# Optimization experiments

Measured on AMD Instinct MI355X. Metric: run time of the kernel, lower is better.

Reference implementation:

```python
import jax, jax.numpy as jnp
import numpy as np

WS = 2   # window_size
NH = 8   # num_heads


def window_attn(x, Wqkv, bqkv, scale, ws=WS, nh=NH):
    # x: (B, H, W, C) -> tiny ws*ws-token windowed MHA, faithful to torch reshape order
    B, H, W, C = x.shape
    hg, wg = H // ws, W // ws
    hd = C // nh
    xw = x.reshape(B, hg, ws, wg, ws, C).transpose(0, 1, 3, 2, 4, 5)  # (B,hg,wg,ws,ws,C)
    qkv = (xw @ Wqkv + bqkv).reshape(B, hg * wg, ws * ws, 3, nh, hd)
    q, k, v = jnp.transpose(qkv, (3, 0, 1, 4, 2, 5))  # each (B,G,nh,n,hd), n=ws*ws
    attn = jax.nn.softmax(jnp.einsum('bgnqd,bgnkd->bgnqk', q, k) * scale, axis=-1)
    o = jnp.einsum('bgnqk,bgnkd->bgnqd', attn, v)
    o = o.transpose(0, 1, 3, 2, 4).reshape(B, hg, wg, ws, ws, C)
    return o.transpose(0, 1, 3, 2, 4, 5).reshape(B, H, W, C)


def reference(x, Wqkv, bqkv, Wproj, bproj):
    B, C, H, W = x.shape
    scale = (C // NH) ** (-0.5)
    xr = x.reshape(B, H, W, C)  # raw reshape (NOT a transpose) -- faithful to source

    # --- Global path ---
    g = window_attn(xr, Wqkv, bqkv, scale) @ Wproj + bproj

    # --- Local path ---
    l = xr.reshape(B, C, H, W)                         # raw reshape, as in source
    l = l.reshape(B, C, H // 2, 2, W // 2, 2).mean(axis=(3, 5))  # AvgPool2d(2)
    h, w = H // 2, W // 2
    l = l.reshape(B, h, w, C)                          # raw reshape, as in source
    l = window_attn(l, Wqkv, bqkv, scale)
    l = l.reshape(B, C, h, w)                          # raw reshape, as in source
    # attn_x: reflect-pad top by 1, AvgPool2d((2,1), stride=1)
    px = jnp.pad(l, ((0, 0), (0, 0), (1, 0), (0, 0)), mode='reflect')
    lx = 0.5 * (px[:, :, :-1, :] + px[:, :, 1:, :])
    # attn_y: reflect-pad right by 1, AvgPool2d((1,2), stride=1)
    py = jnp.pad(l, ((0, 0), (0, 0), (0, 0), (0, 1)), mode='reflect')
    ly = 0.5 * (py[..., :-1] + py[..., 1:])
    # bilinear upsample x2, align_corners=False (half-pixel, matches jax.image.resize)
    l = jax.image.resize(lx + ly, (B, C, H, W), method='bilinear')
    l = l.reshape(B, H, W, C)                          # raw reshape, as in source

    return (g + l).transpose(0, 3, 1, 2)  # (B, C, H, W)


def setup_inputs() -> dict:
    key = jax.random.key(0)
    k1, k2, k3, k4, k5 = jax.random.split(key, 5)
    B, C, H, W = 4, 512, 128, 128
    x = jax.random.normal(k1, (B, C, H, W), dtype=jnp.float32)
    Wqkv = jax.random.normal(k2, (C, 3 * C), dtype=jnp.float32) * 0.02
    bqkv = jax.random.normal(k3, (3 * C,), dtype=jnp.float32) * 0.02
    Wproj = jax.random.normal(k4, (C, C), dtype=jnp.float32) * 0.02
    bproj = jax.random.normal(k5, (C,), dtype=jnp.float32) * 0.02
    return {'x': x, 'Wqkv': Wqkv, 'bqkv': bqkv, 'Wproj': Wproj, 'bproj': bproj}
```

## Files before the change

kernel.cpp:

```cpp
#include <hip/hip_runtime.h>

typedef float f32x4 __attribute__((ext_vector_type(4)));
typedef float f32x2 __attribute__((ext_vector_type(2)));
typedef __bf16 bf16x8 __attribute__((ext_vector_type(8)));
typedef __bf16 bf16x4 __attribute__((ext_vector_type(4)));

__device__ __forceinline__ void gll16(const void* g, void* l) {
  __builtin_amdgcn_global_load_lds(
      (const __attribute__((address_space(1))) uint32_t*)g,
      (__attribute__((address_space(3))) uint32_t*)l, 16, 0, 0);
}

__global__ __launch_bounds__(256) void gemm_bf16_k512(
    const __bf16* __restrict__ A, const __bf16* __restrict__ BT,
    const float* __restrict__ bias, __bf16* __restrict__ C, int N, int gx)
{
  __shared__ __bf16 As[2][8192];
  __shared__ __bf16 Bs[2][8192];
  const int tid = threadIdx.x;
  const int wave = tid >> 6, lane = tid & 63;
  const int wr = (wave >> 1) * 64, wc = (wave & 1) * 64;
  const int l15 = lane & 15, l4 = lane >> 4;

  int lin = blockIdx.x;
  int olin = (lin & 7) * ((int)gridDim.x >> 3) + (lin >> 3);
  int bn = olin % gx, bm = olin / gx;
  const long arow0 = (long)bm * 128;
  const long brow0 = (long)bn * 128;

  const int srow = wave * 8 + (lane >> 3);
  const int scp8 = (lane & 7) * 8;

  f32x4 acc[4][4] = {};

  auto stage = [&](int p, int kt) {
    #pragma unroll
    for (int i = 0; i < 4; i++) {
      int row = srow + i * 32;
      int gc = scp8 ^ ((row & 7) * 8);
      gll16(A  + (arow0 + row) * 512 + kt + gc, (char*)As[p] + i * 4096 + wave * 1024);
      gll16(BT + (brow0 + row) * 512 + kt + gc, (char*)Bs[p] + i * 4096 + wave * 1024);
    }
  };

  stage(0, 0);
  __syncthreads();

  for (int t = 0; t < 8; t++) {
    int cur = t & 1;
    if (t < 7) stage(cur ^ 1, (t + 1) * 64);
    #pragma unroll
    for (int kk = 0; kk < 2; kk++) {
      bf16x8 af[4], bfr[4];
      #pragma unroll
      for (int m = 0; m < 4; m++) {
        int row = wr + m * 16 + l15;
        int cp8 = ((kk * 4 + l4) * 8) ^ ((row & 7) * 8);
        af[m] = *(const bf16x8*)&As[cur][row * 64 + cp8];
      }
      #pragma unroll
      for (int n = 0; n < 4; n++) {
        int row = wc + n * 16 + l15;
        int cp8 = ((kk * 4 + l4) * 8) ^ ((row & 7) * 8);
        bfr[n] = *(const bf16x8*)&Bs[cur][row * 64 + cp8];
      }
      #pragma unroll
      for (int m = 0; m < 4; m++)
        #pragma unroll
        for (int n = 0; n < 4; n++)
          acc[m][n] = __builtin_amdgcn_mfma_f32_16x16x32_bf16(bfr[n], af[m], acc[m][n], 0, 0, 0);
    }
    if (t < 7) __syncthreads();
  }

  #pragma unroll
  for (int m = 0; m < 4; m++) {
    long row = arow0 + wr + m * 16 + l15;
    __bf16* crow = C + row * (long)N + brow0;
    #pragma unroll
    for (int n = 0; n < 4; n++) {
      f32x4 bv = *(const f32x4*)(bias + brow0 + wc + n * 16 + l4 * 4);
      bf16x4 o;
      #pragma unroll
      for (int k = 0; k < 4; k++) o[k] = (__bf16)(acc[m][n][k] + bv[k]);
      *(bf16x4*)(crow + wc + n * 16 + l4 * 4) = o;
    }
  }
}

__global__ __launch_bounds__(256) void attn4(
    const __bf16* __restrict__ qkv, __bf16* __restrict__ o,
    int nwin, int wg, int Wimg, int wpb, int bst)
{
  int tid = blockIdx.x * 256 + threadIdx.x;
  int m = tid & 3;
  int head = (tid >> 2) & 7;
  int win = tid >> 5;
  if (win >= nwin) return;
  int b = win / wpb, wrm = win % wpb;
  int i = wrm / wg, j = wrm % wg;
  int t0 = b * bst + 2 * i * Wimg + 2 * j;
  int tn[4] = { t0, t0 + 1, t0 + Wimg, t0 + Wimg + 1 };
  int trow = tn[m];
  const int co = head * 64;

  float qf[64];
  #pragma unroll
  for (int c = 0; c < 8; c++) {
    bf16x8 v = *(const bf16x8*)(qkv + (long)trow * 1536 + co + c * 8);
    #pragma unroll
    for (int e = 0; e < 8; e++) qf[c * 8 + e] = (float)v[e];
  }

  float s[4];
  #pragma unroll
  for (int n = 0; n < 4; n++) {
    float acc = 0.f;
    #pragma unroll
    for (int c = 0; c < 8; c++) {
      bf16x8 kv = *(const bf16x8*)(qkv + (long)tn[n] * 1536 + 512 + co + c * 8);
      #pragma unroll
      for (int e = 0; e < 8; e++) acc += qf[c * 8 + e] * (float)kv[e];
    }
    s[n] = acc * 0.125f;
  }

  float mx = fmaxf(fmaxf(s[0], s[1]), fmaxf(s[2], s[3]));
  float e0 = __expf(s[0] - mx), e1 = __expf(s[1] - mx),
        e2 = __expf(s[2] - mx), e3 = __expf(s[3] - mx);
  float inv = 1.f / (e0 + e1 + e2 + e3);
  float w4[4] = { e0 * inv, e1 * inv, e2 * inv, e3 * inv };

  float of[64] = {};
  #pragma unroll
  for (int n = 0; n < 4; n++) {
    float wn = w4[n];
    #pragma unroll
    for (int c = 0; c < 8; c++) {
      bf16x8 vv = *(const bf16x8*)(qkv + (long)tn[n] * 1536 + 1024 + co + c * 8);
      #pragma unroll
      for (int e = 0; e < 8; e++) of[c * 8 + e] += wn * (float)vv[e];
    }
  }

  #pragma unroll
  for (int c = 0; c < 8; c++) {
    bf16x8 ov;
    #pragma unroll
    for (int e = 0; e < 8; e++) ov[e] = (__bf16)of[c * 8 + e];
    *(bf16x8*)(o + (long)trow * 512 + co + c * 8) = ov;
  }
}

__global__ __launch_bounds__(256) void transpose_f32_bf16(
    const float* __restrict__ in, __bf16* __restrict__ out, int K, int N)
{
  __shared__ float t[64][65];
  int n0 = blockIdx.x * 64, k0 = blockIdx.y * 64;
  int tid = threadIdx.x;
  int nl4 = (tid & 15) * 4, kl = tid >> 4;
  #pragma unroll
  for (int p = 0; p < 4; p++) {
    int kk = kl + p * 16;
    f32x4 v = *(const f32x4*)(in + (long)(k0 + kk) * N + n0 + nl4);
    t[kk][nl4 + 0] = v.x; t[kk][nl4 + 1] = v.y; t[kk][nl4 + 2] = v.z; t[kk][nl4 + 3] = v.w;
  }
  __syncthreads();
  int ks = tid & 63, wv = tid >> 6;
  #pragma unroll
  for (int p = 0; p < 16; p++) {
    int nn = wv * 16 + p;
    out[(long)(n0 + nn) * K + k0 + ks] = (__bf16)t[ks][nn];
  }
}

__global__ __launch_bounds__(256) void convpool(const float* __restrict__ x,
    __bf16* __restrict__ Xbf, __bf16* __restrict__ P)
{
  int t = blockIdx.x * 256 + threadIdx.x;
  int j8 = (t & 15) * 8;
  int i2 = (t >> 4) & 63;
  long bc = t >> 10;
  const float* r0 = x + bc * 16384 + (2 * i2) * 128 + j8;
  f32x4 a0 = *(const f32x4*)r0,         a1 = *(const f32x4*)(r0 + 4);
  f32x4 b0 = *(const f32x4*)(r0 + 128), b1 = *(const f32x4*)(r0 + 132);
  bf16x8 xa, xb;
  xa[0] = (__bf16)a0.x; xa[1] = (__bf16)a0.y; xa[2] = (__bf16)a0.z; xa[3] = (__bf16)a0.w;
  xa[4] = (__bf16)a1.x; xa[5] = (__bf16)a1.y; xa[6] = (__bf16)a1.z; xa[7] = (__bf16)a1.w;
  xb[0] = (__bf16)b0.x; xb[1] = (__bf16)b0.y; xb[2] = (__bf16)b0.z; xb[3] = (__bf16)b0.w;
  xb[4] = (__bf16)b1.x; xb[5] = (__bf16)b1.y; xb[6] = (__bf16)b1.z; xb[7] = (__bf16)b1.w;
  *(bf16x8*)(Xbf + bc * 16384 + (2 * i2) * 128 + j8) = xa;
  *(bf16x8*)(Xbf + bc * 16384 + (2 * i2) * 128 + 128 + j8) = xb;
  bf16x4 p;
  p[0] = (__bf16)((a0.x + a0.y + b0.x + b0.y) * 0.25f);
  p[1] = (__bf16)((a0.z + a0.w + b0.z + b0.w) * 0.25f);
  p[2] = (__bf16)((a1.x + a1.y + b1.x + b1.y) * 0.25f);
  p[3] = (__bf16)((a1.z + a1.w + b1.z + b1.w) * 0.25f);
  *(bf16x4*)(P + bc * 4096 + i2 * 64 + (t & 15) * 4) = p;
}

__global__ void skern(const __bf16* __restrict__ l, float* __restrict__ s)
{
  int tid = blockIdx.x * 256 + threadIdx.x;
  int j = tid & 63, i = (tid >> 6) & 63;
  long bc = tid >> 12;
  const __bf16* base = l + bc * 4096;
  int im1 = (i == 0) ? 1 : i - 1;
  int jp1 = (j == 63) ? 62 : j + 1;
  float v = 0.5f * (float)base[im1 * 64 + j] + (float)base[i * 64 + j]
          + 0.5f * (float)base[i * 64 + jp1];
  s[tid] = v;
}

__global__ __launch_bounds__(256) void final_v2(
    const __bf16* __restrict__ G, const float* __restrict__ S, float* __restrict__ out)
{
  __shared__ float Sl[8192];
  __shared__ float t[64][65];
  int b = blockIdx.z;
  int p0 = blockIdx.y * 64, c0 = blockIdx.x * 64;
  int tid = threadIdx.x;

  int k2 = blockIdx.y;
  const float* Sb = S + (long)b * 2097152 + (long)k2 * 8192;
  #pragma unroll
  for (int i = 0; i < 8; i++)
    *(f32x4*)&Sl[i * 1024 + tid * 4] = *(const f32x4*)(Sb + i * 1024 + tid * 4);
  __syncthreads();

  int cl4 = (tid & 15) * 4, pl = tid >> 4;
  const __bf16* Gb = G + ((long)b * 16384 + p0) * 512 + c0;
  #pragma unroll
  for (int q2 = 0; q2 < 4; q2++) {
    int pp = pl + q2 * 16;
    bf16x4 g = *(const bf16x4*)(Gb + (long)pp * 512 + cl4);
    int qbase = (p0 + pp) * 512 + c0 + cl4;
    #pragma unroll
    for (int e = 0; e < 4; e++) {
      int q = qbase + e;
      int lc = (q >> 14) & 1;
      int r = q & 16383, hh = r >> 7, ww = r & 127;
      const float* sb = Sl + lc * 4096;
      int i0, i1, j0, j1; float wi0, wi1, wj0, wj1;
      if (hh & 1) { i0 = hh >> 1; i1 = (i0 < 63) ? i0 + 1 : 63; wi0 = 0.75f; wi1 = 0.25f; }
      else        { i1 = hh >> 1; i0 = (i1 > 0) ? i1 - 1 : 0;   wi0 = 0.25f; wi1 = 0.75f; }
      if (ww & 1) { j0 = ww >> 1; j1 = (j0 < 63) ? j0 + 1 : 63; wj0 = 0.75f; wj1 = 0.25f; }
      else        { j1 = ww >> 1; j0 = (j1 > 0) ? j1 - 1 : 0;   wj0 = 0.25f; wj1 = 0.75f; }
      float up = wi0 * (wj0 * sb[i0 * 64 + j0] + wj1 * sb[i0 * 64 + j1])
               + wi1 * (wj0 * sb[i1 * 64 + j0] + wj1 * sb[i1 * 64 + j1]);
      t[pp][cl4 + e] = (float)g[e] + up;
    }
  }
  __syncthreads();
  int l15b = tid & 15, hi = (tid >> 4) & 3, wv = tid >> 6;
  float* ob = out + (long)b * 8388608 + (long)c0 * 16384 + p0;
  #pragma unroll
  for (int it = 0; it < 4; it++) {
    int cc = wv * 16 + it * 4 + hi;
    f32x4 v;
    v.x = t[l15b * 4 + 0][cc]; v.y = t[l15b * 4 + 1][cc];
    v.z = t[l15b * 4 + 2][cc]; v.w = t[l15b * 4 + 3][cc];
    *(f32x4*)(ob + (long)cc * 16384 + l15b * 4) = v;
  }
}

extern "C" void kernel_launch(void* const* d_in, const int* in_sizes, int n_in,
                              void* d_out, int out_size, void* d_ws, size_t ws_size,
                              hipStream_t stream)
{
  const float* x     = (const float*)d_in[0];
  const float* Wqkv  = (const float*)d_in[1];
  const float* bqkv  = (const float*)d_in[2];
  const float* Wproj = (const float*)d_in[3];
  const float* bproj = (const float*)d_in[4];
  float* out = (float*)d_out;

  char* w = (char*)d_ws;
  __bf16* WqkvT  = (__bf16*)w;  w += (size_t)1536 * 512 * 2;
  __bf16* WprojT = (__bf16*)w;  w += (size_t)512 * 512 * 2;
  __bf16* Xbf    = (__bf16*)w;  w += (size_t)65536 * 512 * 2;
  __bf16* G      = Xbf;
  __bf16* P      = (__bf16*)w;  w += (size_t)2048 * 4096 * 2;

  bool batched = ws_size >= ((size_t)356 << 20);
  size_t mchunk = batched ? 65536 : 16384;
  __bf16* QKVbuf = (__bf16*)w;  w += mchunk * 1536 * 2;
  __bf16* Obuf   = (__bf16*)w;
  float*  S      = (float*)QKVbuf;

  transpose_f32_bf16<<<dim3(24, 8), 256, 0, stream>>>(Wqkv, WqkvT, 512, 1536);
  transpose_f32_bf16<<<dim3(8, 8), 256, 0, stream>>>(Wproj, WprojT, 512, 512);
  convpool<<<8192, 256, 0, stream>>>(x, Xbf, P);

  int nch = batched ? 1 : 4;
  int mrows = (int)mchunk;
  for (int c = 0; c < nch; c++) {
    const __bf16* Ac = Xbf + (size_t)c * 16384 * 512;
    gemm_bf16_k512<<<12 * (mrows / 128), 256, 0, stream>>>(Ac, WqkvT, bqkv, QKVbuf, 1536, 12);
    attn4<<<(mrows / 4) * 32 / 256, 256, 0, stream>>>(
        QKVbuf, Obuf, mrows / 4, 64, 128, 4096, 16384);
    gemm_bf16_k512<<<4 * (mrows / 128), 256, 0, stream>>>(
        Obuf, WprojT, bproj, G + (size_t)c * 16384 * 512, 512, 4);
  }

  gemm_bf16_k512<<<12 * 128, 256, 0, stream>>>(P, WqkvT, bqkv, QKVbuf, 1536, 12);
  attn4<<<512, 256, 0, stream>>>(QKVbuf, Obuf, 4096, 32, 64, 1024, 4096);
  skern<<<8388608 / 256, 256, 0, stream>>>(Obuf, S);

  final_v2<<<dim3(8, 256, 4), 256, 0, stream>>>(G, S, out);
}
```

Baseline: 493.1 us.

## Triple-buffer GEMM LDS with 32-wide K tiles and explicit vmcnt waits

Changes the bf16 GEMM main loop from double-buffered 64-wide K tiles to triple-buffered 32-wide K tiles. Loads are issued two stages ahead, with explicit s_waitcnt vmcnt counts and raw s_barrier calls instead of __syncthreads. This is meant to hide global-to-LDS load latency behind MFMA work. The LDS swizzle pattern is redone for the new 32-column row layout. The cost is twice as many barriers per K sweep and more fragile hand-written wait counts.

```diff
diff --git a/kernel.cpp b/kernel.cpp
--- a/kernel.cpp
+++ b/kernel.cpp
@@ -15,8 +15,8 @@
     const __bf16* __restrict__ A, const __bf16* __restrict__ BT,
     const float* __restrict__ bias, __bf16* __restrict__ C, int N, int gx)
 {
-  __shared__ __bf16 As[2][8192];
-  __shared__ __bf16 Bs[2][8192];
+  __shared__ __bf16 As[3][4096];
+  __shared__ __bf16 Bs[3][4096];
   const int tid = threadIdx.x;
   const int wave = tid >> 6, lane = tid & 63;
   const int wr = (wave >> 1) * 64, wc = (wave & 1) * 64;
@@ -28,49 +28,55 @@
   const long arow0 = (long)bm * 128;
   const long brow0 = (long)bn * 128;
 
-  const int srow = wave * 8 + (lane >> 3);
-  const int scp8 = (lane & 7) * 8;
+  const int srow = wave * 16 + (lane >> 2);
+  const int sgc8 = ((lane & 3) ^ (lane >> 4)) * 8;
 
   f32x4 acc[4][4] = {};
 
   auto stage = [&](int p, int kt) {
     #pragma unroll
-    for (int i = 0; i < 4; i++) {
-      int row = srow + i * 32;
-      int gc = scp8 ^ ((row & 7) * 8);
-      gll16(A  + (arow0 + row) * 512 + kt + gc, (char*)As[p] + i * 4096 + wave * 1024);
-      gll16(BT + (brow0 + row) * 512 + kt + gc, (char*)Bs[p] + i * 4096 + wave * 1024);
+    for (int i = 0; i < 2; i++) {
+      int row = srow + i * 64;
+      gll16(A  + (arow0 + row) * 512 + kt + sgc8, (char*)As[p] + i * 4096 + wave * 1024);
+      gll16(BT + (brow0 + row) * 512 + kt + sgc8, (char*)Bs[p] + i * 4096 + wave * 1024);
     }
   };
 
   stage(0, 0);
-  __syncthreads();
-
-  for (int t = 0; t < 8; t++) {
-    int cur = t & 1;
-    if (t < 7) stage(cur ^ 1, (t + 1) * 64);
-    #pragma unroll
-    for (int kk = 0; kk < 2; kk++) {
-      bf16x8 af[4], bfr[4];
+  stage(1, 32);
+
+  const int rs = l15 >> 2;
+  for (int t = 0; t < 16; t++) {
+    if (t > 0) {
+      __builtin_amdgcn_sched_barrier(0);
+      __builtin_amdgcn_s_barrier();
+      __builtin_amdgcn_sched_barrier(0);
+    }
+    if (t + 2 < 16) stage((t + 2) % 3, (t + 2) * 32);
+    if (t < 14)      asm volatile("s_waitcnt vmcnt(8)" ::: "memory");
+    else if (t == 14) asm volatile("s_waitcnt vmcnt(4)" ::: "memory");
+    else              asm volatile("s_waitcnt vmcnt(0)" ::: "memory");
+    __builtin_amdgcn_s_barrier();
+    __builtin_amdgcn_sched_barrier(0);
+
+    const __bf16* as = As[t % 3];
+    const __bf16* bs = Bs[t % 3];
+    bf16x8 af[4], bfr[4];
+    #pragma unroll
+    for (int m = 0; m < 4; m++) {
+      int row = wr + m * 16 + l15;
+      af[m] = *(const bf16x8*)&as[row * 32 + ((l4 ^ rs) * 8)];
+    }
+    #pragma unroll
+    for (int n = 0; n < 4; n++) {
+      int row = wc + n * 16 + l15;
+      bfr[n] = *(const bf16x8*)&bs[row * 32 + ((l4 ^ rs) * 8)];
+    }
+    #pragma unroll
+    for (int m = 0; m < 4; m++)
       #pragma unroll
-      for (int m = 0; m < 4; m++) {
-        int row = wr + m * 16 + l15;
-        int cp8 = ((kk * 4 + l4) * 8) ^ ((row & 7) * 8);
-        af[m] = *(const bf16x8*)&As[cur][row * 64 + cp8];
-      }
-      #pragma unroll
-      for (int n = 0; n < 4; n++) {
-        int row = wc + n * 16 + l15;
-        int cp8 = ((kk * 4 + l4) * 8) ^ ((row & 7) * 8);
-        bfr[n] = *(const bf16x8*)&Bs[cur][row * 64 + cp8];
-      }
-      #pragma unroll
-      for (int m = 0; m < 4; m++)
-        #pragma unroll
-        for (int n = 0; n < 4; n++)
-          acc[m][n] = __builtin_amdgcn_mfma_f32_16x16x32_bf16(bfr[n], af[m], acc[m][n], 0, 0, 0);
-    }
-    if (t < 7) __syncthreads();
+      for (int n = 0; n < 4; n++)
+        acc[m][n] = __builtin_amdgcn_mfma_f32_16x16x32_bf16(bfr[n], af[m], acc[m][n], 0, 0, 0);
   }
 
   #pragma unroll
```

After: 482.6 us. -2.1%, faster.
